# Optimization experiments

Hardware: AMD Instinct MI355X
Metric: run time of the kernel (lower is better)

The kernel has to match this reference:

```python
import jax, jax.numpy as jnp
import numpy as np

N_NODES = 100000
N_EDGES = 3200000
D_IN = 256
D_OUT = 256


def setup_inputs() -> dict:
    key = jax.random.key(0)
    k1, k2, k3, k4, k5 = jax.random.split(key, 5)
    input_feature = jax.random.normal(k1, (N_NODES, D_IN), dtype=jnp.float32)
    edge_row = jax.random.randint(k2, (N_EDGES,), 0, N_NODES, dtype=jnp.int32)
    edge_col = jax.random.randint(k3, (N_EDGES,), 0, N_NODES, dtype=jnp.int32)
    edge_val = jax.random.uniform(k4, (N_EDGES,), dtype=jnp.float32)
    # xavier_uniform for weight [D_IN, D_OUT]
    limit = float(np.sqrt(6.0 / (D_IN + D_OUT)))
    weight = jax.random.uniform(k5, (D_IN, D_OUT), minval=-limit, maxval=limit, dtype=jnp.float32)
    bias = jnp.zeros((D_OUT,), dtype=jnp.float32)
    return {
        "input_feature": input_feature,
        "edge_row": edge_row,
        "edge_col": edge_col,
        "edge_val": edge_val,
        "weight": weight,
        "bias": bias,
    }


def reference(input_feature, edge_row, edge_col, edge_val, weight, bias):
    # support = X @ W   [N, D_OUT]
    support = input_feature @ weight
    # output[i] = sum_{(i,j) in E} A[i,j] * support[j]  (sparse adjacency SpMM)
    messages = edge_val[:, None] * support[edge_col]  # [E, D_OUT]
    output = jax.ops.segment_sum(messages, edge_row, num_segments=N_NODES)
    return output + bias
```

## Files before the change

kernel.cpp:

```cpp
#include <hip/hip_runtime.h>

#define N_NODES 100000
#define N_EDGES 3200000
#define DIM 256

#define BROWS 128
#define NBUCK 782
#define CAP   5120

typedef short short8 __attribute__((ext_vector_type(8)));
typedef float f32x4 __attribute__((ext_vector_type(4)));

static __device__ __forceinline__ unsigned short f2bf(float f) {
    unsigned int u = __float_as_uint(f);
    u = (u + 0x7FFFu + ((u >> 16) & 1u)) >> 16;
    return (unsigned short)u;
}

__global__ __launch_bounds__(512) void k_bucket2(const int* __restrict__ row,
                                                 const int* __restrict__ col,
                                                 const float* __restrict__ val,
                                                 int* __restrict__ bcur,
                                                 int2* __restrict__ tmp) {
    __shared__ int hist[NBUCK];
    __shared__ int base[NBUCK];
    int t = threadIdx.x;
    const int per = N_EDGES / 256;
    int e0 = blockIdx.x * per, e1 = e0 + per;
    for (int i = t; i < NBUCK; i += 512) hist[i] = 0;
    __syncthreads();
    for (int e = e0 + t; e < e1; e += 512)
        atomicAdd(&hist[row[e] >> 7], 1);
    __syncthreads();
    for (int i = t; i < NBUCK; i += 512) {
        int c = hist[i];
        base[i] = c ? (i * CAP + atomicAdd(&bcur[i], c)) : 0;
        hist[i] = 0;
    }
    __syncthreads();
    for (int e = e0 + t; e < e1; e += 512) {
        int r = row[e];
        int b = r >> 7;
        int off = atomicAdd(&hist[b], 1);
        tmp[base[b] + off] = make_int2(((r & 127) << 17) | col[e],
                                       __float_as_int(val[e]));
    }
}

__global__ __launch_bounds__(1024) void k_place3(const int* __restrict__ bcur,
                                                 const int2* __restrict__ tmp,
                                                 int2* __restrict__ csr,
                                                 int* __restrict__ rs,
                                                 int* __restrict__ re,
                                                 int* __restrict__ gcur) {
    __shared__ int h[BROWS];
    __shared__ int cur[BROWS];
    __shared__ int gb;
    int t = threadIdx.x;
    int b = blockIdx.x;
    int cnt = bcur[b];
    const int2* tb = tmp + (size_t)b * CAP;
    if (t < BROWS) h[t] = 0;
    __syncthreads();
    for (int i = t; i < cnt; i += 1024)
        atomicAdd(&h[(tb[i].x >> 17) & 127], 1);
    __syncthreads();
    int x = (t < BROWS) ? h[t] : 0;
    __syncthreads();
    for (int off = 1; off < BROWS; off <<= 1) {
        int v = (t >= off && t < BROWS) ? h[t - off] : 0;
        __syncthreads();
        if (t < BROWS) h[t] += v;
        __syncthreads();
    }
    if (t == 0) gb = atomicAdd(gcur, cnt);
    __syncthreads();
    if (t < BROWS) {
        int inc = h[t];
        int ex = gb + inc - x;
        cur[t] = ex;
        int rr = b * BROWS + t;
        if (rr < N_NODES) { rs[rr] = ex; re[rr] = gb + inc; }
    }
    __syncthreads();
    for (int i = t; i < cnt; i += 1024) {
        int2 rec = tb[i];
        int p = atomicAdd(&cur[(rec.x >> 17) & 127], 1);
        csr[p] = make_int2(rec.x & 0x1FFFF, rec.y);
    }
}

__global__ void k_wpack(const float* __restrict__ W, unsigned short* __restrict__ wp) {
    int t = blockIdx.x * 256 + threadIdx.x;
    int lane = t & 63;
    int nt = (t >> 6) & 15;
    int kc = t >> 10;
    int n = nt * 16 + (lane & 15);
    int kbase = kc * 32 + ((lane >> 4) << 3);
    unsigned short* dst = wp + (size_t)t * 8;
#pragma unroll
    for (int j = 0; j < 8; j++) dst[j] = f2bf(W[(size_t)(kbase + j) * DIM + n]);
}

#define LDSTRIDE 528
__global__ __launch_bounds__(1024, 4) void k_gemm(const float* __restrict__ X,
                                                  const unsigned short* __restrict__ wp,
                                                  unsigned short* __restrict__ sup) {
    __shared__ char pool[16 * 16 * LDSTRIDE];
    unsigned short* wlds = (unsigned short*)pool;
    int t = threadIdx.x;
    int wave = t >> 6, lane = t & 63;
    int q = lane >> 4, nl = lane & 15;

    const int nstrips = (N_NODES + 255) / 256;
    for (int s = blockIdx.x; s < nstrips; s += gridDim.x) {
        for (int i = t; i < 8192; i += 1024)
            ((uint4*)wlds)[i] = ((const uint4*)wp)[i];
        __syncthreads();

        int rowbase = s * 256 + wave * 16;
        f32x4 acc[16];
#pragma unroll
        for (int mt = 0; mt < 16; mt++) acc[mt] = (f32x4){0.f, 0.f, 0.f, 0.f};

        for (int kc = 0; kc < 8; kc++) {
            int r = rowbase + nl;
            short8 b = (short8)0;
            if (r < N_NODES) {
                const float* bp = X + (size_t)r * DIM + kc * 32 + (q << 3);
                float4 b0 = *(const float4*)bp;
                float4 b1 = *(const float4*)(bp + 4);
                b[0] = (short)f2bf(b0.x); b[1] = (short)f2bf(b0.y);
                b[2] = (short)f2bf(b0.z); b[3] = (short)f2bf(b0.w);
                b[4] = (short)f2bf(b1.x); b[5] = (short)f2bf(b1.y);
                b[6] = (short)f2bf(b1.z); b[7] = (short)f2bf(b1.w);
            }
#pragma unroll
            for (int mt = 0; mt < 16; mt++) {
                short8 a = *(const short8*)&wlds[(size_t)(((kc * 16 + mt) * 64) + lane) * 8];
                acc[mt] = __builtin_amdgcn_mfma_f32_16x16x32_bf16(a, b, acc[mt], 0, 0, 0);
            }
        }
        __syncthreads();

        char* wbase = pool + wave * (16 * LDSTRIDE);
#pragma unroll
        for (int mt = 0; mt < 16; mt++) {
            uint2 p;
            p.x = ((unsigned int)f2bf(acc[mt][1]) << 16) | f2bf(acc[mt][0]);
            p.y = ((unsigned int)f2bf(acc[mt][3]) << 16) | f2bf(acc[mt][2]);
            *(uint2*)(wbase + nl * LDSTRIDE + mt * 32 + q * 8) = p;
        }
#pragma unroll
        for (int i = 0; i < 8; i++) {
            int row = 2 * i + (lane >> 5);
            uint4 v = *(const uint4*)(wbase + row * LDSTRIDE + (lane & 31) * 16);
            int node = rowbase + row;
            if (node < N_NODES)
                *(uint4*)((char*)sup + (size_t)node * 512 + (lane & 31) * 16) = v;
        }
        __syncthreads();
    }
}

__global__ __launch_bounds__(256) void k_agg(const int* __restrict__ rs,
                                             const int* __restrict__ re,
                                             const int2* __restrict__ csr,
                                             const unsigned short* __restrict__ sup,
                                             const float* __restrict__ bias,
                                             float* __restrict__ out) {
    int wave = threadIdx.x >> 6, lane = threadIdx.x & 63;
    int r = blockIdx.x * 4 + wave;
    int s = rs[r], e = re[r];
    int g = lane >> 4;
    int L = lane & 15;

    float acc[16];
#pragma unroll
    for (int j = 0; j < 16; j++) acc[j] = 0.f;

    int i = s;
    for (; i + 4 <= e; i += 4) {
        int2 ce = csr[i + g];
        float v = __int_as_float(ce.y);
        const uint4* sp = (const uint4*)(sup + (size_t)ce.x * DIM + L * 16);
        uint4 u0 = sp[0];
        uint4 u1 = sp[1];
        unsigned int uu[8] = {u0.x, u0.y, u0.z, u0.w, u1.x, u1.y, u1.z, u1.w};
#pragma unroll
        for (int k = 0; k < 8; k++) {
            acc[2 * k]     += v * __uint_as_float(uu[k] << 16);
            acc[2 * k + 1] += v * __uint_as_float(uu[k] & 0xFFFF0000u);
        }
    }
    {
        int idx = i + g;
        if (idx < e) {
            int2 ce = csr[idx];
            float v = __int_as_float(ce.y);
            const uint4* sp = (const uint4*)(sup + (size_t)ce.x * DIM + L * 16);
            uint4 u0 = sp[0];
            uint4 u1 = sp[1];
            unsigned int uu[8] = {u0.x, u0.y, u0.z, u0.w, u1.x, u1.y, u1.z, u1.w};
#pragma unroll
            for (int k = 0; k < 8; k++) {
                acc[2 * k]     += v * __uint_as_float(uu[k] << 16);
                acc[2 * k + 1] += v * __uint_as_float(uu[k] & 0xFFFF0000u);
            }
        }
    }
#pragma unroll
    for (int j = 0; j < 16; j++) {
        float x = acc[j];
        x += __shfl_down(x, 32, 64);
        x += __shfl_down(x, 16, 64);
        acc[j] = x;
    }
    if (lane < 16) {
        float4* op = (float4*)(out + (size_t)r * DIM + L * 16);
        const float4* bp = (const float4*)(bias + L * 16);
#pragma unroll
        for (int qq = 0; qq < 4; qq++) {
            float4 b = bp[qq];
            float4 o;
            o.x = acc[4 * qq]     + b.x;
            o.y = acc[4 * qq + 1] + b.y;
            o.z = acc[4 * qq + 2] + b.z;
            o.w = acc[4 * qq + 3] + b.w;
            op[qq] = o;
        }
    }
}

extern "C" void kernel_launch(void* const* d_in, const int* in_sizes, int n_in,
                              void* d_out, int out_size, void* d_ws, size_t ws_size,
                              hipStream_t stream) {
    const float* X    = (const float*)d_in[0];
    const int*   erow = (const int*)d_in[1];
    const int*   ecol = (const int*)d_in[2];
    const float* eval = (const float*)d_in[3];
    const float* W    = (const float*)d_in[4];
    const float* bias = (const float*)d_in[5];
    float* out = (float*)d_out;

    char* ws = (char*)d_ws;
    int*            rs    = (int*)ws;
    int*            re    = (int*)(ws + 409600);
    int*            bcur  = (int*)(ws + 819200);
    int*            gcur  = (int*)(ws + 822400);
    unsigned short* wp    = (unsigned short*)(ws + 823296);
    int2*           csr   = (int2*)(ws + 954368);
    unsigned short* sup   = (unsigned short*)(ws + 26554368);
    int2*           tmp   = (int2*)(ws + 26554368);

    hipMemsetAsync(bcur, 0, 4096, stream);
    k_bucket2<<<256, 512, 0, stream>>>(erow, ecol, eval, bcur, tmp);
    k_place3<<<NBUCK, 1024, 0, stream>>>(bcur, tmp, csr, rs, re, gcur);
    k_wpack<<<32, 256, 0, stream>>>(W, wp);
    k_gemm<<<256, 1024, 0, stream>>>(X, wp, sup);
    k_agg<<<N_NODES / 4, 256, 0, stream>>>(rs, re, csr, sup, bias, out);
}
```

Before: 552.2 us.

## Split aggregation into two column-half passes and double bucketing blocks

```diff
diff --git a/kernel.cpp b/kernel.cpp
--- a/kernel.cpp
+++ b/kernel.cpp
@@ -25,7 +25,7 @@
     __shared__ int hist[NBUCK];
     __shared__ int base[NBUCK];
     int t = threadIdx.x;
-    const int per = N_EDGES / 256;
+    const int per = N_EDGES / 512;
     int e0 = blockIdx.x * per, e1 = e0 + per;
     for (int i = t; i < NBUCK; i += 512) hist[i] = 0;
     __syncthreads();
@@ -163,64 +163,68 @@
     }
 }
 
-__global__ __launch_bounds__(256) void k_agg(const int* __restrict__ rs,
-                                             const int* __restrict__ re,
-                                             const int2* __restrict__ csr,
-                                             const unsigned short* __restrict__ sup,
-                                             const float* __restrict__ bias,
-                                             float* __restrict__ out) {
+static __device__ __forceinline__ void fma8(float* acc, float v, uint4 u) {
+    unsigned int uu[4] = {u.x, u.y, u.z, u.w};
+#pragma unroll
+    for (int k = 0; k < 4; k++) {
+        acc[2 * k]     += v * __uint_as_float(uu[k] << 16);
+        acc[2 * k + 1] += v * __uint_as_float(uu[k] & 0xFFFF0000u);
+    }
+}
+
+__global__ __launch_bounds__(256) void k_agg_half(const int* __restrict__ rs,
+                                                  const int* __restrict__ re,
+                                                  const int2* __restrict__ csr,
+                                                  const unsigned short* __restrict__ sup,
+                                                  const float* __restrict__ bias,
+                                                  float* __restrict__ out,
+                                                  int doff) {
     int wave = threadIdx.x >> 6, lane = threadIdx.x & 63;
     int r = blockIdx.x * 4 + wave;
     int s = rs[r], e = re[r];
     int g = lane >> 4;
     int L = lane & 15;
 
-    float acc[16];
-#pragma unroll
-    for (int j = 0; j < 16; j++) acc[j] = 0.f;
+    float acc[8];
+#pragma unroll
+    for (int j = 0; j < 8; j++) acc[j] = 0.f;
 
     int i = s;
+    for (; i + 8 <= e; i += 8) {
+        int2 ce0 = csr[i + g];
+        int2 ce1 = csr[i + 4 + g];
+        const uint4* sp0 = (const uint4*)(sup + (size_t)ce0.x * DIM + doff + L * 8);
+        const uint4* sp1 = (const uint4*)(sup + (size_t)ce1.x * DIM + doff + L * 8);
+        uint4 u0 = *sp0;
+        uint4 u1 = *sp1;
+        fma8(acc, __int_as_float(ce0.y), u0);
+        fma8(acc, __int_as_float(ce1.y), u1);
+    }
     for (; i + 4 <= e; i += 4) {
         int2 ce = csr[i + g];
-        float v = __int_as_float(ce.y);
-        const uint4* sp = (const uint4*)(sup + (size_t)ce.x * DIM + L * 16);
-        uint4 u0 = sp[0];
-        uint4 u1 = sp[1];
-        unsigned int uu[8] = {u0.x, u0.y, u0.z, u0.w, u1.x, u1.y, u1.z, u1.w};
-#pragma unroll
-        for (int k = 0; k < 8; k++) {
-            acc[2 * k]     += v * __uint_as_float(uu[k] << 16);
-            acc[2 * k + 1] += v * __uint_as_float(uu[k] & 0xFFFF0000u);
-        }
+        uint4 u = *(const uint4*)(sup + (size_t)ce.x * DIM + doff + L * 8);
+        fma8(acc, __int_as_float(ce.y), u);
     }
     {
         int idx = i + g;
         if (idx < e) {
             int2 ce = csr[idx];
-            float v = __int_as_float(ce.y);
-            const uint4* sp = (const uint4*)(sup + (size_t)ce.x * DIM + L * 16);
-            uint4 u0 = sp[0];
-            uint4 u1 = sp[1];
-            unsigned int uu[8] = {u0.x, u0.y, u0.z, u0.w, u1.x, u1.y, u1.z, u1.w};
-#pragma unroll
-            for (int k = 0; k < 8; k++) {
-                acc[2 * k]     += v * __uint_as_float(uu[k] << 16);
-                acc[2 * k + 1] += v * __uint_as_float(uu[k] & 0xFFFF0000u);
-            }
-        }
-    }
-#pragma unroll
-    for (int j = 0; j < 16; j++) {
+            uint4 u = *(const uint4*)(sup + (size_t)ce.x * DIM + doff + L * 8);
+            fma8(acc, __int_as_float(ce.y), u);
+        }
+    }
+#pragma unroll
+    for (int j = 0; j < 8; j++) {
         float x = acc[j];
         x += __shfl_down(x, 32, 64);
         x += __shfl_down(x, 16, 64);
         acc[j] = x;
     }
     if (lane < 16) {
-        float4* op = (float4*)(out + (size_t)r * DIM + L * 16);
-        const float4* bp = (const float4*)(bias + L * 16);
-#pragma unroll
-        for (int qq = 0; qq < 4; qq++) {
+        float4* op = (float4*)(out + (size_t)r * DIM + doff + L * 8);
+        const float4* bp = (const float4*)(bias + doff + L * 8);
+#pragma unroll
+        for (int qq = 0; qq < 2; qq++) {
             float4 b = bp[qq];
             float4 o;
             o.x = acc[4 * qq]     + b.x;
@@ -254,9 +258,10 @@
     int2*           tmp   = (int2*)(ws + 26554368);
 
     hipMemsetAsync(bcur, 0, 4096, stream);
-    k_bucket2<<<256, 512, 0, stream>>>(erow, ecol, eval, bcur, tmp);
+    k_bucket2<<<512, 512, 0, stream>>>(erow, ecol, eval, bcur, tmp);
     k_place3<<<NBUCK, 1024, 0, stream>>>(bcur, tmp, csr, rs, re, gcur);
     k_wpack<<<32, 256, 0, stream>>>(W, wp);
     k_gemm<<<256, 1024, 0, stream>>>(X, wp, sup);
-    k_agg<<<N_NODES / 4, 256, 0, stream>>>(rs, re, csr, sup, bias, out);
-}
+    k_agg_half<<<N_NODES / 4, 256, 0, stream>>>(rs, re, csr, sup, bias, out, 0);
+    k_agg_half<<<N_NODES / 4, 256, 0, stream>>>(rs, re, csr, sup, bias, out, 128);
+}
```

New measurement: 554.6 us. About the same (+0.4%).
